# Kernel tuning notes

Measured on AMD Instinct MI355X. Metric: run time of the kernel, lower is better.

The kernel has to match this reference:

```python
import jax, jax.numpy as jnp
import numpy as np

E = 8          # n_experts
TOP_K = 2      # n_active_experts


def setup_inputs() -> dict:
    key = jax.random.key(0)
    ks = jax.random.split(key, 9)
    B, S, D, H = 4, 2048, 2048, 1408
    w = 0.02  # weight scale for numerical stability
    return {
        "x": jax.random.normal(ks[0], (B, S, D), dtype=jnp.float32),
        "gate_w": jax.random.normal(ks[1], (E, D), dtype=jnp.float32) * w,
        "expert_bias": jnp.zeros((E,), dtype=jnp.float32),
        "Wg": jax.random.normal(ks[2], (E, H, D), dtype=jnp.float32) * w,
        "Wu": jax.random.normal(ks[3], (E, H, D), dtype=jnp.float32) * w,
        "Wd": jax.random.normal(ks[4], (E, D, H), dtype=jnp.float32) * w,
        "Ws_g": jax.random.normal(ks[5], (H, D), dtype=jnp.float32) * w,
        "Ws_u": jax.random.normal(ks[6], (H, D), dtype=jnp.float32) * w,
        "Ws_d": jax.random.normal(ks[7], (D, H), dtype=jnp.float32) * w,
    }


def _swiglu(x, wg, wu, wd):
    # torch Linear layout: y = x @ W.T
    return (jax.nn.silu(x @ wg.T) * (x @ wu.T)) @ wd.T


def reference(x, gate_w, expert_bias, Wg, Wu, Wd, Ws_g, Ws_u, Ws_d):
    B, S, D = x.shape
    flat = x.reshape(-1, D)                      # [N, D]
    N = flat.shape[0]

    logits = flat @ gate_w.T                     # [N, E]
    probs = jax.nn.softmax(logits, axis=-1)
    biased = logits + expert_bias
    _, top_idx = jax.lax.top_k(biased, TOP_K)    # [N, K] (bias used only for selection)
    top_w = jnp.take_along_axis(probs, top_idx, axis=-1)
    top_w = top_w / jnp.sum(top_w, axis=-1, keepdims=True)

    # dense per-token combine weights: cw[n, e] = sum_k top_w[n,k] * (top_idx[n,k]==e)
    rows = jnp.arange(N)[:, None]
    cw = jnp.zeros((N, E), dtype=flat.dtype).at[rows, top_idx].add(top_w)

    out = jnp.zeros_like(flat)
    for e in range(E):  # fixed small expert count; equivalent to gather/scatter dispatch
        out = out + cw[:, e:e + 1] * _swiglu(flat, Wg[e], Wu[e], Wd[e])

    out = out + _swiglu(flat, Ws_g, Ws_u, Ws_d)  # shared expert
    return out.reshape(B, S, D)
```

## Files before the change

### kernel.cpp

```cpp
#include <hip/hip_runtime.h>
#include <hip/hip_bf16.h>

#define N_TOK 8192
#define DDIM  2048
#define HDIM  1408
#define ROWS_R 16384
#define ROWS_T 24576
#define MAXTILES 104
#define BM 256
#define BK 32

typedef unsigned short u16;
typedef unsigned int   u32;
typedef __bf16 bf16x8 __attribute__((ext_vector_type(8)));
typedef float  f32x4  __attribute__((ext_vector_type(4)));

__device__ __forceinline__ u16 f2bf(float f) {
  union { float f; u32 u; } v; v.f = f;
  u32 u = v.u;
  return (u16)((u + 0x7fffu + ((u >> 16) & 1u)) >> 16);
}
__device__ __forceinline__ float bf2f(u16 b) {
  union { u32 u; float f; } v; v.u = ((u32)b) << 16; return v.f;
}

typedef __attribute__((address_space(1))) void gvoid;
typedef __attribute__((address_space(3))) void lvoid;
__device__ __forceinline__ void gload16(const void* g, void* l) {
  __builtin_amdgcn_global_load_lds((gvoid*)g, (lvoid*)l, 16, 0, 0);
}

#define BAR __builtin_amdgcn_s_barrier()
#define SP1 __builtin_amdgcn_s_setprio(1)
#define SP0 __builtin_amdgcn_s_setprio(0)
#define LGK0 do { asm volatile("s_waitcnt lgkmcnt(0)" ::: "memory"); \
                  __builtin_amdgcn_sched_barrier(0); } while (0)
#define VMCNT(n) asm volatile("s_waitcnt vmcnt(" #n ")" ::: "memory")

#define FSW(r) ((((r) & 3) ^ (((r) >> 2) & 3)))

__global__ void k_gate(const float* __restrict__ x, const float* __restrict__ gw,
                       const float* __restrict__ bias, int* __restrict__ tok_idx,
                       float* __restrict__ wts, int* __restrict__ counts,
                       u16* __restrict__ xb) {
  int lane = threadIdx.x & 63;
  int n = blockIdx.x * 4 + (threadIdx.x >> 6);
  const float* xr = x + (size_t)n * DDIM;
  u16* xbr = xb + (size_t)n * DDIM;
  float acc[8];
#pragma unroll
  for (int e = 0; e < 8; ++e) acc[e] = 0.f;
#pragma unroll 2
  for (int j0 = 0; j0 < DDIM; j0 += 256) {
    float4 xv = *(const float4*)(xr + j0 + lane * 4);
    u32 p0 = (u32)f2bf(xv.x) | ((u32)f2bf(xv.y) << 16);
    u32 p1 = (u32)f2bf(xv.z) | ((u32)f2bf(xv.w) << 16);
    *(uint2*)(xbr + j0 + lane * 4) = make_uint2(p0, p1);
#pragma unroll
    for (int e = 0; e < 8; ++e) {
      float4 gv = *(const float4*)(gw + e * DDIM + j0 + lane * 4);
      acc[e] += xv.x * gv.x + xv.y * gv.y + xv.z * gv.z + xv.w * gv.w;
    }
  }
#pragma unroll
  for (int e = 0; e < 8; ++e) {
#pragma unroll
    for (int off = 32; off > 0; off >>= 1) acc[e] += __shfl_xor(acc[e], off);
  }
  if (lane == 0) {
    float m = acc[0];
    for (int e = 1; e < 8; ++e) m = fmaxf(m, acc[e]);
    float p[8];
    for (int e = 0; e < 8; ++e) p[e] = expf(acc[e] - m);
    float b0[8];
    for (int e = 0; e < 8; ++e) b0[e] = acc[e] + bias[e];
    int i0 = 0;
    for (int e = 1; e < 8; ++e) if (b0[e] > b0[i0]) i0 = e;
    int i1 = (i0 == 0) ? 1 : 0;
    for (int e = 0; e < 8; ++e) if (e != i0 && b0[e] > b0[i1]) i1 = e;
    float w0 = p[i0], w1 = p[i1], inv = 1.f / (w0 + w1);
    tok_idx[2 * n] = i0; tok_idx[2 * n + 1] = i1;
    wts[2 * n] = w0 * inv; wts[2 * n + 1] = w1 * inv;
    atomicAdd(&counts[i0], 1); atomicAdd(&counts[i1], 1);
  }
}

__global__ void k_scan(const int* __restrict__ counts, int* __restrict__ offsets,
                       int* __restrict__ cursors, int* __restrict__ ntiles,
                       int4* __restrict__ tiles) {
  if (threadIdx.x != 0 || blockIdx.x != 0) return;
  int off = 0, idx = 0;
  for (int e = 0; e < 8; ++e) {
    offsets[e] = off; cursors[e] = 0;
    int T = counts[e];
    for (int r = 0; r < T; r += BM) {
      int nr = T - r; if (nr > BM) nr = BM;
      tiles[idx++] = make_int4(e, off + r, nr, 0);
    }
    off += T;
  }
  offsets[8] = off;
  for (int r = 0; r < N_TOK; r += BM)
    tiles[idx++] = make_int4(8, ROWS_R + r, BM, 0);
  *ntiles = idx;
}

__global__ void k_build(const int* __restrict__ tok_idx, const int* __restrict__ offsets,
                        int* __restrict__ cursors, int* __restrict__ token_ids,
                        int* __restrict__ pos) {
  int n = blockIdx.x * blockDim.x + threadIdx.x;
  if (n >= N_TOK) return;
#pragma unroll
  for (int s = 0; s < 2; ++s) {
    int e = tok_idx[2 * n + s];
    int p = offsets[e] + atomicAdd(&cursors[e], 1);
    token_ids[p] = n;
    pos[2 * n + s] = p;
  }
  token_ids[ROWS_R + n] = n;
}

__global__ void k_convall(const float* __restrict__ Wg, const float* __restrict__ Wsg,
                          const float* __restrict__ Wu, const float* __restrict__ Wsu,
                          const float* __restrict__ Wd, const float* __restrict__ Wsd,
                          u16* __restrict__ wgb, u16* __restrict__ wub, u16* __restrict__ wdb) {
  const long PER = (long)9 * HDIM * DDIM / 8;
  const long BIG = (long)8 * HDIM * DDIM / 8;
  const long TOT = 3 * PER;
  long stride = (long)gridDim.x * blockDim.x;
  for (long i = (long)blockIdx.x * blockDim.x + threadIdx.x; i < TOT; i += stride) {
    int g = (int)(i / PER);
    long r = i - (long)g * PER;
    const float* src; u16* dst;
    if (g == 0)      { dst = wgb; src = (r < BIG) ? Wg + r * 8 : Wsg + (r - BIG) * 8; }
    else if (g == 1) { dst = wub; src = (r < BIG) ? Wu + r * 8 : Wsu + (r - BIG) * 8; }
    else             { dst = wdb; src = (r < BIG) ? Wd + r * 8 : Wsd + (r - BIG) * 8; }
    float4 a = ((const float4*)src)[0], b = ((const float4*)src)[1];
    u32 p0 = (u32)f2bf(a.x) | ((u32)f2bf(a.y) << 16);
    u32 p1 = (u32)f2bf(a.z) | ((u32)f2bf(a.w) << 16);
    u32 p2 = (u32)f2bf(b.x) | ((u32)f2bf(b.y) << 16);
    u32 p3 = (u32)f2bf(b.z) | ((u32)f2bf(b.w) << 16);
    ((uint4*)dst)[r] = make_uint4(p0, p1, p2, p3);
  }
}

__global__ __launch_bounds__(512, 2) void k_gemm1(
    const u16* __restrict__ xb, const u16* __restrict__ wgb,
    const int* __restrict__ token_ids, const int* __restrict__ ntiles,
    const int4* __restrict__ tiles, u16* __restrict__ h) {
  __shared__ u16 As[4][BM * BK];
  __shared__ u16 Bgs[4][128 * BK];
  __shared__ u16 Bus[4][128 * BK];

  int ntl = *ntiles;
  int nwg = (HDIM / 128) * ntl;
  int bid = blockIdx.x;
  if (bid >= nwg) return;
  int q8 = nwg >> 3, r8 = nwg & 7;
  int xcd = bid & 7, pp = bid >> 3;
  int lid = (xcd < r8 ? xcd * (q8 + 1) : r8 * (q8 + 1) + (xcd - r8) * q8) + pp;
  int bx = lid / ntl, tile = lid - bx * ntl;

  int4 tl = tiles[tile];
  int set = tl.x, grow = tl.y, nrows = tl.z;

  int t = threadIdx.x;
  int wid = t >> 6, lane = t & 63;
  int wr = wid >> 1, wc = wid & 1;
  int l15 = lane & 15, lhi = lane >> 4;

  const u16* aptr[2];
#pragma unroll
  for (int i = 0; i < 2; ++i) {
    int chunk = i * 512 + t;
    int r = chunk >> 2, cc = chunk & 3;
    int c = cc ^ FSW(r);
    int rr = r < nrows ? r : nrows - 1;
    int tok = token_ids[grow + rr];
    aptr[i] = xb + (size_t)tok * DDIM + c * 8;
  }
  const u16* gptr;
  {
    int r = t >> 2, cc = t & 3;
    int c = cc ^ FSW(r);
    gptr = wgb + (size_t)set * (HDIM * DDIM) + (size_t)(bx * 128 + r) * DDIM + c * 8;
  }
  const size_t WUOFF = (size_t)9 * HDIM * DDIM;

#define G1_ISSUE(b, k0) { \
  gload16(aptr[0] + (k0), (char*)As[b] + (size_t)t * 16); \
  gload16(aptr[1] + (k0), (char*)As[b] + (size_t)(512 + t) * 16); \
  gload16(gptr + (k0), (char*)Bgs[b] + (size_t)t * 16); \
  gload16(gptr + WUOFF + (k0), (char*)Bus[b] + (size_t)t * 16); }

#define G1_BODY(b) { \
  bf16x8 a0[2], a1[2], bg[4], bu[4]; \
  _Pragma("unroll") for (int n_ = 0; n_ < 4; ++n_) { \
    int r_ = wc * 64 + n_ * 16 + l15; \
    int off_ = r_ * 64 + ((lhi ^ FSW(r_)) * 16); \
    bg[n_] = *(const bf16x8*)((const char*)Bgs[b] + off_); \
    bu[n_] = *(const bf16x8*)((const char*)Bus[b] + off_); } \
  _Pragma("unroll") for (int m_ = 0; m_ < 2; ++m_) { \
    int r_ = wr * 32 + m_ * 16 + l15; \
    a0[m_] = *(const bf16x8*)((const char*)As[b] + r_ * 64 + ((lhi ^ FSW(r_)) * 16)); } \
  LGK0; SP1; \
  _Pragma("unroll") for (int m_ = 0; m_ < 2; ++m_) \
  _Pragma("unroll") for (int n_ = 0; n_ < 4; ++n_) { \
    accg[m_][n_] = __builtin_amdgcn_mfma_f32_16x16x32_bf16(a0[m_], bg[n_], accg[m_][n_], 0, 0, 0); \
    accu[m_][n_] = __builtin_amdgcn_mfma_f32_16x16x32_bf16(a0[m_], bu[n_], accu[m_][n_], 0, 0, 0); } \
  SP0; \
  _Pragma("unroll") for (int m_ = 0; m_ < 2; ++m_) { \
    int r_ = 128 + wr * 32 + m_ * 16 + l15; \
    a1[m_] = *(const bf16x8*)((const char*)As[b] + r_ * 64 + ((lhi ^ FSW(r_)) * 16)); } \
  LGK0; SP1; \
  _Pragma("unroll") for (int m_ = 0; m_ < 2; ++m_) \
  _Pragma("unroll") for (int n_ = 0; n_ < 4; ++n_) { \
    accg[2 + m_][n_] = __builtin_amdgcn_mfma_f32_16x16x32_bf16(a1[m_], bg[n_], accg[2 + m_][n_], 0, 0, 0); \
    accu[2 + m_][n_] = __builtin_amdgcn_mfma_f32_16x16x32_bf16(a1[m_], bu[n_], accu[2 + m_][n_], 0, 0, 0); } \
  SP0; }

  f32x4 accg[4][4], accu[4][4];
  f32x4 z = {0.f, 0.f, 0.f, 0.f};
#pragma unroll
  for (int m = 0; m < 4; ++m)
#pragma unroll
    for (int n = 0; n < 4; ++n) { accg[m][n] = z; accu[m][n] = z; }

  const int NK = DDIM / BK;

  VMCNT(0);
  G1_ISSUE(0, 0); G1_ISSUE(1, BK); G1_ISSUE(2, 2 * BK);
  VMCNT(8); BAR;

  for (int kt = 0; kt < NK - 3; ++kt) {
    G1_ISSUE((kt + 3) & 3, (kt + 3) * BK);
    G1_BODY(kt & 3);
    VMCNT(8); BAR;
  }
  G1_BODY((NK - 3) & 3); VMCNT(4); BAR;
  G1_BODY((NK - 2) & 3); VMCNT(0); BAR;
  G1_BODY((NK - 1) & 3);

#pragma unroll
  for (int m = 0; m < 4; ++m) {
#pragma unroll
    for (int n = 0; n < 4; ++n) {
      int col = bx * 128 + wc * 64 + n * 16 + l15;
#pragma unroll
      for (int qq = 0; qq < 4; ++qq) {
        int rl = (m >> 1) * 128 + wr * 32 + (m & 1) * 16 + lhi * 4 + qq;
        if (rl < nrows) {
          float g = accg[m][n][qq], u = accu[m][n][qq];
          float hv = g / (1.f + expf(-g)) * u;
          h[(size_t)(grow + rl) * HDIM + col] = f2bf(hv);
        }
      }
    }
  }
#undef G1_ISSUE
#undef G1_BODY
}

__global__ __launch_bounds__(512, 2) void k_gemm2(
    const u16* __restrict__ h, const u16* __restrict__ wdb,
    const int* __restrict__ ntiles, const int4* __restrict__ tiles,
    u16* __restrict__ y) {
  __shared__ u16 As2[4][BM * BK];
  __shared__ u16 Bs2[4][256 * BK];

  int ntl = *ntiles;
  int nwg = (DDIM / 256) * ntl;
  int bid = blockIdx.x;
  if (bid >= nwg) return;
  int q8 = nwg >> 3, r8 = nwg & 7;
  int xcd = bid & 7, pp = bid >> 3;
  int lid = (xcd < r8 ? xcd * (q8 + 1) : r8 * (q8 + 1) + (xcd - r8) * q8) + pp;
  int bx = lid / ntl, tile = lid - bx * ntl;

  int4 tl = tiles[tile];
  int set = tl.x, grow = tl.y, nrows = tl.z;

  int t = threadIdx.x;
  int wid = t >> 6, lane = t & 63;
  int wr = wid >> 2, wc = wid & 3;
  int l15 = lane & 15, lhi = lane >> 4;

  const u16* aptr[2];
  const u16* bptr[2];
#pragma unroll
  for (int i = 0; i < 2; ++i) {
    int chunk = i * 512 + t;
    int r = chunk >> 2, cc = chunk & 3;
    int c = cc ^ FSW(r);
    aptr[i] = h + (size_t)(grow + r) * HDIM + c * 8;
    bptr[i] = wdb + (size_t)set * (DDIM * HDIM) + (size_t)(bx * 256 + r) * HDIM + c * 8;
  }

#define G2_ISSUE(b, k0) { \
  gload16(aptr[0] + (k0), (char*)As2[b] + (size_t)t * 16); \
  gload16(aptr[1] + (k0), (char*)As2[b] + (size_t)(512 + t) * 16); \
  gload16(bptr[0] + (k0), (char*)Bs2[b] + (size_t)t * 16); \
  gload16(bptr[1] + (k0), (char*)Bs2[b] + (size_t)(512 + t) * 16); }

#define G2_BODY(b) { \
  bf16x8 af[4], bf[4]; \
  _Pragma("unroll") for (int n_ = 0; n_ < 4; ++n_) { \
    int r_ = wc * 64 + n_ * 16 + l15; \
    bf[n_] = *(const bf16x8*)((const char*)Bs2[b] + r_ * 64 + ((lhi ^ FSW(r_)) * 16)); } \
  _Pragma("unroll") for (int m_ = 0; m_ < 4; ++m_) { \
    int r_ = wr * 128 + m_ * 16 + l15; \
    af[m_] = *(const bf16x8*)((const char*)As2[b] + r_ * 64 + ((lhi ^ FSW(r_)) * 16)); } \
  LGK0; SP1; \
  _Pragma("unroll") for (int m_ = 0; m_ < 4; ++m_) \
  _Pragma("unroll") for (int n_ = 0; n_ < 4; ++n_) \
    acc[m_][n_] = __builtin_amdgcn_mfma_f32_16x16x32_bf16(af[m_], bf[n_], acc[m_][n_], 0, 0, 0); \
  SP0; \
  _Pragma("unroll") for (int m_ = 0; m_ < 4; ++m_) { \
    int r_ = wr * 128 + (4 + m_) * 16 + l15; \
    af[m_] = *(const bf16x8*)((const char*)As2[b] + r_ * 64 + ((lhi ^ FSW(r_)) * 16)); } \
  LGK0; SP1; \
  _Pragma("unroll") for (int m_ = 0; m_ < 4; ++m_) \
  _Pragma("unroll") for (int n_ = 0; n_ < 4; ++n_) \
    acc[4 + m_][n_] = __builtin_amdgcn_mfma_f32_16x16x32_bf16(af[m_], bf[n_], acc[4 + m_][n_], 0, 0, 0); \
  SP0; }

  f32x4 acc[8][4];
  f32x4 z = {0.f, 0.f, 0.f, 0.f};
#pragma unroll
  for (int m = 0; m < 8; ++m)
#pragma unroll
    for (int n = 0; n < 4; ++n) acc[m][n] = z;

  const int NK2 = HDIM / BK;

  VMCNT(0);
  G2_ISSUE(0, 0); G2_ISSUE(1, BK); G2_ISSUE(2, 2 * BK);
  VMCNT(8); BAR;

  for (int kt = 0; kt < NK2 - 3; ++kt) {
    G2_ISSUE((kt + 3) & 3, (kt + 3) * BK);
    G2_BODY(kt & 3);
    VMCNT(8); BAR;
  }
  G2_BODY((NK2 - 3) & 3); VMCNT(4); BAR;
  G2_BODY((NK2 - 2) & 3); VMCNT(0); BAR;
  G2_BODY((NK2 - 1) & 3);

#pragma unroll
  for (int m = 0; m < 8; ++m) {
#pragma unroll
    for (int n = 0; n < 4; ++n) {
      int col = bx * 256 + wc * 64 + n * 16 + l15;
#pragma unroll
      for (int qq = 0; qq < 4; ++qq) {
        int rl = wr * 128 + m * 16 + lhi * 4 + qq;
        if (rl < nrows)
          y[(size_t)(grow + rl) * DDIM + col] = f2bf(acc[m][n][qq]);
      }
    }
  }
#undef G2_ISSUE
#undef G2_BODY
}

__global__ void k_comb(const u16* __restrict__ y, const int* __restrict__ pos,
                       const float* __restrict__ wts, float* __restrict__ out) {
  int n = blockIdx.x;
  int c8 = threadIdx.x;
  int p0 = pos[2 * n], p1 = pos[2 * n + 1];
  float w0 = wts[2 * n], w1 = wts[2 * n + 1];
  uint4 a = ((const uint4*)(y + (size_t)p0 * DDIM))[c8];
  uint4 b = ((const uint4*)(y + (size_t)p1 * DDIM))[c8];
  uint4 c = ((const uint4*)(y + (size_t)(ROWS_R + n) * DDIM))[c8];
  float* o = out + (size_t)n * DDIM + c8 * 8;
#pragma unroll
  for (int j = 0; j < 4; ++j) {
    u32 ua = ((const u32*)&a)[j], ub = ((const u32*)&b)[j], uc = ((const u32*)&c)[j];
    o[2 * j]     = w0 * bf2f((u16)(ua & 0xffff)) + w1 * bf2f((u16)(ub & 0xffff)) + bf2f((u16)(uc & 0xffff));
    o[2 * j + 1] = w0 * bf2f((u16)(ua >> 16))    + w1 * bf2f((u16)(ub >> 16))    + bf2f((u16)(uc >> 16));
  }
}

extern "C" void kernel_launch(void* const* d_in, const int* in_sizes, int n_in,
                              void* d_out, int out_size, void* d_ws, size_t ws_size,
                              hipStream_t stream) {
  const float* x    = (const float*)d_in[0];
  const float* gw   = (const float*)d_in[1];
  const float* bias = (const float*)d_in[2];
  const float* Wg   = (const float*)d_in[3];
  const float* Wu   = (const float*)d_in[4];
  const float* Wd   = (const float*)d_in[5];
  const float* Wsg  = (const float*)d_in[6];
  const float* Wsu  = (const float*)d_in[7];
  const float* Wsd  = (const float*)d_in[8];
  float* out = (float*)d_out;

  char* ws = (char*)d_ws;
  size_t off = 0;
  auto alloc = [&](size_t bytes) -> void* {
    void* p = ws + off;
    off += (bytes + 255) & ~(size_t)255;
    return p;
  };
  u16* xb  = (u16*)alloc((size_t)N_TOK * DDIM * 2);
  u16* wgb = (u16*)alloc((size_t)9 * HDIM * DDIM * 2);
  u16* wub = (u16*)alloc((size_t)9 * HDIM * DDIM * 2);
  u16* wdb = (u16*)alloc((size_t)9 * DDIM * HDIM * 2);
  u16* h   = (u16*)alloc((size_t)ROWS_T * HDIM * 2);
  u16* y   = (u16*)alloc((size_t)ROWS_T * DDIM * 2);
  int*   token_ids = (int*)alloc(ROWS_T * 4);
  int*   tok_idx   = (int*)alloc(N_TOK * 2 * 4);
  int*   pos       = (int*)alloc(N_TOK * 2 * 4);
  float* wts       = (float*)alloc(N_TOK * 2 * 4);
  int*   counts  = (int*)alloc(8 * 4);
  int*   offsets = (int*)alloc(9 * 4);
  int*   cursors = (int*)alloc(8 * 4);
  int*   ntiles  = (int*)alloc(4);
  int4*  tiles   = (int4*)alloc(MAXTILES * 16);

  hipMemsetAsync(counts, 0, 8 * 4, stream);
  k_gate<<<N_TOK / 4, 256, 0, stream>>>(x, gw, bias, tok_idx, wts, counts, xb);
  k_scan<<<1, 64, 0, stream>>>(counts, offsets, cursors, ntiles, tiles);
  k_build<<<(N_TOK + 255) / 256, 256, 0, stream>>>(tok_idx, offsets, cursors, token_ids, pos);

  k_convall<<<4096, 256, 0, stream>>>(Wg, Wsg, Wu, Wsu, Wd, Wsd, wgb, wub, wdb);

  k_gemm1<<<(HDIM / 128) * MAXTILES, 512, 0, stream>>>(xb, wgb, token_ids, ntiles, tiles, h);
  k_gemm2<<<(DDIM / 256) * MAXTILES, 512, 0, stream>>>(h, wdb, ntiles, tiles, y);
  k_comb<<<N_TOK, 256, 0, stream>>>(y, pos, wts, out);
}
```

Before: 1.084 ms.

## Interleave gate/up weights into one B tile and use 128-byte swizzled LDS rows

Gate and up projection rows are now interleaved in 16-row groups into a single 256-row B tile, so gemm1 runs as a uniform 8x4 wave-tile GEMM like gemm2, with the SwiGLU pairing done from adjacent accumulator columns in the epilogue. Both GEMMs switch the LDS layout from 64-byte rows with a 4-way XOR swizzle to 128-byte rows that pack two K-halves, using an 8-way XOR swizzle. The aim is fewer LDS bank conflicts and a shared fragment-load and MFMA schedule for both kernels. The trade-off is more complex address math and a changed per-wave work mapping in gemm1.

Result: faster. 1.057 ms (-2.5%).

```diff
diff --git a/kernel.cpp b/kernel.cpp
--- a/kernel.cpp
+++ b/kernel.cpp
@@ -37,7 +37,23 @@
                   __builtin_amdgcn_sched_barrier(0); } while (0)
 #define VMCNT(n) asm volatile("s_waitcnt vmcnt(" #n ")" ::: "memory")
 
-#define FSW(r) ((((r) & 3) ^ (((r) >> 2) & 3)))
+
+#define RDA(b, mb, dst) { \
+  _Pragma("unroll") for (int m_ = 0; m_ < 4; ++m_) { \
+    int r_ = wr * 128 + ((mb) + m_) * 16 + l15; \
+    int rp_ = r_ & 127, hb_ = r_ >> 7; \
+    (dst)[m_] = *(const bf16x8*)((const char*)As[b] + rp_ * 128 + ((((hb_ << 2) + lhi) ^ (rp_ & 7)) * 16)); } }
+
+#define RDB(b) { \
+  _Pragma("unroll") for (int n_ = 0; n_ < 4; ++n_) { \
+    int r_ = wc * 64 + n_ * 16 + l15; \
+    int rp_ = r_ & 127, hb_ = r_ >> 7; \
+    bf[n_] = *(const bf16x8*)((const char*)Bs[b] + rp_ * 128 + ((((hb_ << 2) + lhi) ^ (rp_ & 7)) * 16)); } }
+
+#define MMC(mb, AFR) { \
+  _Pragma("unroll") for (int m_ = 0; m_ < 4; ++m_) \
+  _Pragma("unroll") for (int n_ = 0; n_ < 4; ++n_) \
+    acc[(mb) + m_][n_] = __builtin_amdgcn_mfma_f32_16x16x32_bf16((AFR)[m_], bf[n_], acc[(mb) + m_][n_], 0, 0, 0); }
 
 __global__ void k_gate(const float* __restrict__ x, const float* __restrict__ gw,
                        const float* __restrict__ bias, int* __restrict__ tok_idx,
@@ -145,12 +161,11 @@
 }
 
 __global__ __launch_bounds__(512, 2) void k_gemm1(
-    const u16* __restrict__ xb, const u16* __restrict__ wgb,
+    const u16* __restrict__ xb, const u16* __restrict__ wgb, const u16* __restrict__ wub,
     const int* __restrict__ token_ids, const int* __restrict__ ntiles,
     const int4* __restrict__ tiles, u16* __restrict__ h) {
   __shared__ u16 As[4][BM * BK];
-  __shared__ u16 Bgs[4][128 * BK];
-  __shared__ u16 Bus[4][128 * BK];
+  __shared__ u16 Bs[4][BM * BK];
 
   int ntl = *ntiles;
   int nwg = (HDIM / 128) * ntl;
@@ -166,107 +181,87 @@
 
   int t = threadIdx.x;
   int wid = t >> 6, lane = t & 63;
-  int wr = wid >> 1, wc = wid & 1;
+  int wr = wid >> 2, wc = wid & 3;
   int l15 = lane & 15, lhi = lane >> 4;
 
   const u16* aptr[2];
+  const u16* bptr[2];
 #pragma unroll
   for (int i = 0; i < 2; ++i) {
     int chunk = i * 512 + t;
-    int r = chunk >> 2, cc = chunk & 3;
-    int c = cc ^ FSW(r);
-    int rr = r < nrows ? r : nrows - 1;
-    int tok = token_ids[grow + rr];
-    aptr[i] = xb + (size_t)tok * DDIM + c * 8;
-  }
-  const u16* gptr;
-  {
-    int r = t >> 2, cc = t & 3;
-    int c = cc ^ FSW(r);
-    gptr = wgb + (size_t)set * (HDIM * DDIM) + (size_t)(bx * 128 + r) * DDIM + c * 8;
-  }
-  const size_t WUOFF = (size_t)9 * HDIM * DDIM;
-
-#define G1_ISSUE(b, k0) { \
+    int rp = chunk >> 3, sl = chunk & 7;
+    int u = sl ^ (rp & 7);
+    int row = rp + (u >> 2) * 128;
+    int kcol = (u & 3) * 8;
+    int rr = row < nrows ? row : nrows - 1;
+    aptr[i] = xb + (size_t)token_ids[grow + rr] * DDIM + kcol;
+    int group = row >> 4;
+    int wrow = bx * 128 + (group >> 1) * 16 + (row & 15);
+    const u16* bb = (group & 1) ? wub : wgb;
+    bptr[i] = bb + (size_t)set * (HDIM * DDIM) + (size_t)wrow * DDIM + kcol;
+  }
+
+#define STG1(b, k0) { \
   gload16(aptr[0] + (k0), (char*)As[b] + (size_t)t * 16); \
   gload16(aptr[1] + (k0), (char*)As[b] + (size_t)(512 + t) * 16); \
-  gload16(gptr + (k0), (char*)Bgs[b] + (size_t)t * 16); \
-  gload16(gptr + WUOFF + (k0), (char*)Bus[b] + (size_t)t * 16); }
-
-#define G1_BODY(b) { \
-  bf16x8 a0[2], a1[2], bg[4], bu[4]; \
-  _Pragma("unroll") for (int n_ = 0; n_ < 4; ++n_) { \
-    int r_ = wc * 64 + n_ * 16 + l15; \
-    int off_ = r_ * 64 + ((lhi ^ FSW(r_)) * 16); \
-    bg[n_] = *(const bf16x8*)((const char*)Bgs[b] + off_); \
-    bu[n_] = *(const bf16x8*)((const char*)Bus[b] + off_); } \
-  _Pragma("unroll") for (int m_ = 0; m_ < 2; ++m_) { \
-    int r_ = wr * 32 + m_ * 16 + l15; \
-    a0[m_] = *(const bf16x8*)((const char*)As[b] + r_ * 64 + ((lhi ^ FSW(r_)) * 16)); } \
-  LGK0; SP1; \
-  _Pragma("unroll") for (int m_ = 0; m_ < 2; ++m_) \
-  _Pragma("unroll") for (int n_ = 0; n_ < 4; ++n_) { \
-    accg[m_][n_] = __builtin_amdgcn_mfma_f32_16x16x32_bf16(a0[m_], bg[n_], accg[m_][n_], 0, 0, 0); \
-    accu[m_][n_] = __builtin_amdgcn_mfma_f32_16x16x32_bf16(a0[m_], bu[n_], accu[m_][n_], 0, 0, 0); } \
-  SP0; \
-  _Pragma("unroll") for (int m_ = 0; m_ < 2; ++m_) { \
-    int r_ = 128 + wr * 32 + m_ * 16 + l15; \
-    a1[m_] = *(const bf16x8*)((const char*)As[b] + r_ * 64 + ((lhi ^ FSW(r_)) * 16)); } \
-  LGK0; SP1; \
-  _Pragma("unroll") for (int m_ = 0; m_ < 2; ++m_) \
-  _Pragma("unroll") for (int n_ = 0; n_ < 4; ++n_) { \
-    accg[2 + m_][n_] = __builtin_amdgcn_mfma_f32_16x16x32_bf16(a1[m_], bg[n_], accg[2 + m_][n_], 0, 0, 0); \
-    accu[2 + m_][n_] = __builtin_amdgcn_mfma_f32_16x16x32_bf16(a1[m_], bu[n_], accu[2 + m_][n_], 0, 0, 0); } \
-  SP0; }
-
-  f32x4 accg[4][4], accu[4][4];
+  gload16(bptr[0] + (k0), (char*)Bs[b] + (size_t)t * 16); \
+  gload16(bptr[1] + (k0), (char*)Bs[b] + (size_t)(512 + t) * 16); }
+
+#define BODY1(b) { \
+  bf16x8 af0[4], af1[4], bf[4]; \
+  RDB(b); RDA(b, 0, af0); \
+  LGK0; SP1; MMC(0, af0); SP0; \
+  RDA(b, 4, af1); \
+  LGK0; SP1; MMC(4, af1); SP0; }
+
+  f32x4 acc[8][4];
   f32x4 z = {0.f, 0.f, 0.f, 0.f};
 #pragma unroll
-  for (int m = 0; m < 4; ++m)
-#pragma unroll
-    for (int n = 0; n < 4; ++n) { accg[m][n] = z; accu[m][n] = z; }
+  for (int m = 0; m < 8; ++m)
+#pragma unroll
+    for (int n = 0; n < 4; ++n) acc[m][n] = z;
 
   const int NK = DDIM / BK;
 
   VMCNT(0);
-  G1_ISSUE(0, 0); G1_ISSUE(1, BK); G1_ISSUE(2, 2 * BK);
+  STG1(0, 0); STG1(1, BK); STG1(2, 2 * BK);
   VMCNT(8); BAR;
 
-  for (int kt = 0; kt < NK - 3; ++kt) {
-    G1_ISSUE((kt + 3) & 3, (kt + 3) * BK);
-    G1_BODY(kt & 3);
+  for (int kt = 0; kt <= NK - 4; ++kt) {
+    STG1((kt + 3) & 3, (kt + 3) * BK);
+    BODY1(kt & 3);
     VMCNT(8); BAR;
   }
-  G1_BODY((NK - 3) & 3); VMCNT(4); BAR;
-  G1_BODY((NK - 2) & 3); VMCNT(0); BAR;
-  G1_BODY((NK - 1) & 3);
-
-#pragma unroll
-  for (int m = 0; m < 4; ++m) {
-#pragma unroll
-    for (int n = 0; n < 4; ++n) {
-      int col = bx * 128 + wc * 64 + n * 16 + l15;
+  BODY1((NK - 3) & 3); VMCNT(4); BAR;
+  BODY1((NK - 2) & 3); VMCNT(0); BAR;
+  BODY1((NK - 1) & 3);
+
+#pragma unroll
+  for (int m = 0; m < 8; ++m) {
+#pragma unroll
+    for (int j = 0; j < 2; ++j) {
+      int col = bx * 128 + (wc * 2 + j) * 16 + l15;
 #pragma unroll
       for (int qq = 0; qq < 4; ++qq) {
-        int rl = (m >> 1) * 128 + wr * 32 + (m & 1) * 16 + lhi * 4 + qq;
+        int rl = wr * 128 + m * 16 + lhi * 4 + qq;
         if (rl < nrows) {
-          float g = accg[m][n][qq], u = accu[m][n][qq];
+          float g = acc[m][2 * j][qq], u = acc[m][2 * j + 1][qq];
           float hv = g / (1.f + expf(-g)) * u;
           h[(size_t)(grow + rl) * HDIM + col] = f2bf(hv);
         }
       }
     }
   }
-#undef G1_ISSUE
-#undef G1_BODY
+#undef STG1
+#undef BODY1
 }
 
 __global__ __launch_bounds__(512, 2) void k_gemm2(
     const u16* __restrict__ h, const u16* __restrict__ wdb,
     const int* __restrict__ ntiles, const int4* __restrict__ tiles,
     u16* __restrict__ y) {
-  __shared__ u16 As2[4][BM * BK];
-  __shared__ u16 Bs2[4][256 * BK];
+  __shared__ u16 As[4][BM * BK];
+  __shared__ u16 Bs[4][BM * BK];
 
   int ntl = *ntiles;
   int nwg = (DDIM / 256) * ntl;
@@ -290,39 +285,26 @@
 #pragma unroll
   for (int i = 0; i < 2; ++i) {
     int chunk = i * 512 + t;
-    int r = chunk >> 2, cc = chunk & 3;
-    int c = cc ^ FSW(r);
-    aptr[i] = h + (size_t)(grow + r) * HDIM + c * 8;
-    bptr[i] = wdb + (size_t)set * (DDIM * HDIM) + (size_t)(bx * 256 + r) * HDIM + c * 8;
-  }
-
-#define G2_ISSUE(b, k0) { \
-  gload16(aptr[0] + (k0), (char*)As2[b] + (size_t)t * 16); \
-  gload16(aptr[1] + (k0), (char*)As2[b] + (size_t)(512 + t) * 16); \
-  gload16(bptr[0] + (k0), (char*)Bs2[b] + (size_t)t * 16); \
-  gload16(bptr[1] + (k0), (char*)Bs2[b] + (size_t)(512 + t) * 16); }
-
-#define G2_BODY(b) { \
-  bf16x8 af[4], bf[4]; \
-  _Pragma("unroll") for (int n_ = 0; n_ < 4; ++n_) { \
-    int r_ = wc * 64 + n_ * 16 + l15; \
-    bf[n_] = *(const bf16x8*)((const char*)Bs2[b] + r_ * 64 + ((lhi ^ FSW(r_)) * 16)); } \
-  _Pragma("unroll") for (int m_ = 0; m_ < 4; ++m_) { \
-    int r_ = wr * 128 + m_ * 16 + l15; \
-    af[m_] = *(const bf16x8*)((const char*)As2[b] + r_ * 64 + ((lhi ^ FSW(r_)) * 16)); } \
-  LGK0; SP1; \
-  _Pragma("unroll") for (int m_ = 0; m_ < 4; ++m_) \
-  _Pragma("unroll") for (int n_ = 0; n_ < 4; ++n_) \
-    acc[m_][n_] = __builtin_amdgcn_mfma_f32_16x16x32_bf16(af[m_], bf[n_], acc[m_][n_], 0, 0, 0); \
-  SP0; \
-  _Pragma("unroll") for (int m_ = 0; m_ < 4; ++m_) { \
-    int r_ = wr * 128 + (4 + m_) * 16 + l15; \
-    af[m_] = *(const bf16x8*)((const char*)As2[b] + r_ * 64 + ((lhi ^ FSW(r_)) * 16)); } \
-  LGK0; SP1; \
-  _Pragma("unroll") for (int m_ = 0; m_ < 4; ++m_) \
-  _Pragma("unroll") for (int n_ = 0; n_ < 4; ++n_) \
-    acc[4 + m_][n_] = __builtin_amdgcn_mfma_f32_16x16x32_bf16(af[m_], bf[n_], acc[4 + m_][n_], 0, 0, 0); \
-  SP0; }
+    int rp = chunk >> 3, sl = chunk & 7;
+    int u = sl ^ (rp & 7);
+    int row = rp + (u >> 2) * 128;
+    int kcol = (u & 3) * 8;
+    aptr[i] = h + (size_t)(grow + row) * HDIM + kcol;
+    bptr[i] = wdb + (size_t)set * (DDIM * HDIM) + (size_t)(bx * 256 + row) * HDIM + kcol;
+  }
+
+#define STG2(b, k0) { \
+  gload16(aptr[0] + (k0), (char*)As[b] + (size_t)t * 16); \
+  gload16(aptr[1] + (k0), (char*)As[b] + (size_t)(512 + t) * 16); \
+  gload16(bptr[0] + (k0), (char*)Bs[b] + (size_t)t * 16); \
+  gload16(bptr[1] + (k0), (char*)Bs[b] + (size_t)(512 + t) * 16); }
+
+#define BODY2(b) { \
+  bf16x8 af0[4], af1[4], bf[4]; \
+  RDB(b); RDA(b, 0, af0); \
+  LGK0; SP1; MMC(0, af0); SP0; \
+  RDA(b, 4, af1); \
+  LGK0; SP1; MMC(4, af1); SP0; }
 
   f32x4 acc[8][4];
   f32x4 z = {0.f, 0.f, 0.f, 0.f};
@@ -334,17 +316,17 @@
   const int NK2 = HDIM / BK;
 
   VMCNT(0);
-  G2_ISSUE(0, 0); G2_ISSUE(1, BK); G2_ISSUE(2, 2 * BK);
+  STG2(0, 0); STG2(1, BK); STG2(2, 2 * BK);
   VMCNT(8); BAR;
 
-  for (int kt = 0; kt < NK2 - 3; ++kt) {
-    G2_ISSUE((kt + 3) & 3, (kt + 3) * BK);
-    G2_BODY(kt & 3);
+  for (int kt = 0; kt <= NK2 - 4; ++kt) {
+    STG2((kt + 3) & 3, (kt + 3) * BK);
+    BODY2(kt & 3);
     VMCNT(8); BAR;
   }
-  G2_BODY((NK2 - 3) & 3); VMCNT(4); BAR;
-  G2_BODY((NK2 - 2) & 3); VMCNT(0); BAR;
-  G2_BODY((NK2 - 1) & 3);
+  BODY2((NK2 - 3) & 3); VMCNT(4); BAR;
+  BODY2((NK2 - 2) & 3); VMCNT(0); BAR;
+  BODY2((NK2 - 1) & 3);
 
 #pragma unroll
   for (int m = 0; m < 8; ++m) {
@@ -359,8 +341,8 @@
       }
     }
   }
-#undef G2_ISSUE
-#undef G2_BODY
+#undef STG2
+#undef BODY2
 }
 
 __global__ void k_comb(const u16* __restrict__ y, const int* __restrict__ pos,
@@ -425,7 +407,7 @@
 
   k_convall<<<4096, 256, 0, stream>>>(Wg, Wsg, Wu, Wsu, Wd, Wsd, wgb, wub, wdb);
 
-  k_gemm1<<<(HDIM / 128) * MAXTILES, 512, 0, stream>>>(xb, wgb, token_ids, ntiles, tiles, h);
+  k_gemm1<<<(HDIM / 128) * MAXTILES, 512, 0, stream>>>(xb, wgb, wub, token_ids, ntiles, tiles, h);
   k_gemm2<<<(DDIM / 256) * MAXTILES, 512, 0, stream>>>(h, wdb, ntiles, tiles, y);
   k_comb<<<N_TOK, 256, 0, stream>>>(y, pos, wts, out);
 }
```
